# Performance work log

Measured on AMD Instinct MI355X. Metric: run time of the kernel, lower is better.

The kernel has to match this reference:

```python
import jax, jax.numpy as jnp
import numpy as np

N_NODES = 50000
N_EDGES = 1600000
D_EDGE = 64
D_NODE = 64
D_HID = 256
D_OUT = 64


def setup_inputs() -> dict:
    key = jax.random.key(0)
    ks = jax.random.split(key, 5)
    node_feats = jax.random.normal(ks[0], (N_NODES, D_NODE), dtype=jnp.float32)
    edge_feats = jax.random.normal(ks[1], (N_EDGES, D_EDGE), dtype=jnp.float32)
    receivers = jax.random.randint(ks[2], (N_EDGES,), 0, N_NODES, dtype=jnp.int64 if jax.config.jax_enable_x64 else jnp.int32)
    W1 = jax.random.normal(ks[3], (D_EDGE + D_NODE, D_HID), dtype=jnp.float32) * 0.05
    b1 = jnp.zeros((D_HID,), dtype=jnp.float32)
    W2 = jax.random.normal(ks[4], (D_HID, D_OUT), dtype=jnp.float32) * 0.05
    b2 = jnp.zeros((D_OUT,), dtype=jnp.float32)
    return {"node_feats": node_feats, "edge_feats": edge_feats, "receivers": receivers,
            "W1": W1, "b1": b1, "W2": W2, "b2": b2}


def reference(node_feats, edge_feats, receivers, W1, b1, W2, b2):
    # e2n aggregation: mean of incoming-edge features per node (segment mean),
    # faithful to gathering edata[G.incoming_edges(nid)] and averaging.
    n = node_feats.shape[0]
    agg_sum = jax.ops.segment_sum(edge_feats, receivers, num_segments=n)  # [N, De]
    counts = jax.ops.segment_sum(jnp.ones((edge_feats.shape[0],), edge_feats.dtype),
                                 receivers, num_segments=n)               # [N]
    agg = agg_sum / jnp.maximum(counts, 1.0)[:, None]
    # concat aggregated edge features with node features, then MLP updater
    x = jnp.concatenate([agg, node_feats], axis=1)                        # [N, De+Dv]
    h = jax.nn.relu(x @ W1 + b1)
    return h @ W2 + b2                                                    # [N, Dout]
```

## Files before the change

### kernel.cpp

```cpp
#include <hip/hip_runtime.h>

#define N_NODES 50000
#define N_EDGES 1600000
#define CAP 160

typedef short bf16x8 __attribute__((ext_vector_type(8)));
typedef float f32x4  __attribute__((ext_vector_type(4)));

__device__ inline unsigned f2bf(float f) {
    union { float f; unsigned u; } v; v.f = f;
    unsigned r = v.u + 0x7fff + ((v.u >> 16) & 1);
    return r >> 16;
}

__global__ __launch_bounds__(256) void zero_cursors_kernel(int* __restrict__ p) {
    int i = blockIdx.x * 256 + threadIdx.x;
    if (i < N_NODES) p[i] = 0;
}

__global__ __launch_bounds__(256) void bin_direct_kernel(
    const int* __restrict__ receivers,
    int* __restrict__ cursors,
    int* __restrict__ edge_ids)
{
    int e = blockIdx.x * 256 + threadIdx.x;
    if (e < N_EDGES) {
        int r = receivers[e];
        int p = atomicAdd(&cursors[r], 1);
        if (p < CAP) edge_ids[(size_t)r * CAP + p] = e;
    }
}

__global__ __launch_bounds__(256) void prepack_kernel(
    const float* __restrict__ W1, const float* __restrict__ W2,
    short* __restrict__ W1p, short* __restrict__ W2p)
{
    int t = blockIdx.x * 256 + threadIdx.x;
    if (t < 4096) {
        int c = (t >> 6) & 3, nt = t >> 8, l = t & 63;
        short tmp[8];
        #pragma unroll
        for (int j = 0; j < 8; ++j) {
            int k = c * 32 + (l >> 4) * 8 + j;
            tmp[j] = (short)f2bf(W1[k * 256 + nt * 16 + (l & 15)]);
        }
        #pragma unroll
        for (int j = 0; j < 8; ++j) W1p[(size_t)t * 8 + j] = tmp[j];
    } else if (t < 6144) {
        int u = t - 4096;
        int c = (u >> 6) & 7, nt = u >> 9, l = u & 63;
        short tmp[8];
        #pragma unroll
        for (int j = 0; j < 8; ++j) {
            int k = c * 32 + (l >> 4) * 8 + j;
            tmp[j] = (short)f2bf(W2[k * 64 + nt * 16 + (l & 15)]);
        }
        #pragma unroll
        for (int j = 0; j < 8; ++j) W2p[(size_t)u * 8 + j] = tmp[j];
    }
}

__global__ __launch_bounds__(512) void fused_gather_mlp_kernel(
    const float* __restrict__ edge_feats,
    const int*   __restrict__ edge_ids,
    const int*   __restrict__ counts,
    const float* __restrict__ node_feats,
    const short* __restrict__ W1p, const float* __restrict__ b1,
    const short* __restrict__ W2p, const float* __restrict__ b2,
    float*       __restrict__ out)
{
    __shared__ uint4 xbuf[512];
    __shared__ uint4 hbuf[1024];
    char* xb = (char*)xbuf;
    char* hb = (char*)hbuf;
    const int t = threadIdx.x;
    const int l = t & 63;
    const int w = t >> 6;
    const int g = l >> 4;
    const int q = l & 15;
    const int node0 = blockIdx.x * 32;

    {
        int node = t >> 4;
        int qq = t & 15;
        int nl = node0 + node;
        float4 v = make_float4(0.f, 0.f, 0.f, 0.f);
        if (nl < N_NODES) v = ((const float4*)(node_feats + (size_t)nl * 64))[qq];
        unsigned lo = f2bf(v.x) | (f2bf(v.y) << 16);
        unsigned hi = f2bf(v.z) | (f2bf(v.w) << 16);
        int byte = node * 256 + 128 + qq * 8;
        byte ^= (node & 7) << 4;
        *(uint2*)(xb + byte) = make_uint2(lo, hi);
    }

    for (int n = 0; n < 4; ++n) {
        int nodeLocal = w * 4 + n;
        int node = node0 + nodeLocal;
        int cnt = (node < N_NODES) ? min(counts[node], CAP) : 0;
        const int* ids = edge_ids + (size_t)node * CAP;
        float4 acc0 = make_float4(0.f, 0.f, 0.f, 0.f);
        float4 acc1 = make_float4(0.f, 0.f, 0.f, 0.f);
        for (int base = 0; base < cnt; base += 64) {
            int m = min(cnt - base, 64);
            int myid = (l < m) ? ids[base + l] : 0;
            for (int half = 0; half < m; half += 32) {
                #pragma unroll
                for (int u = 0; u < 8; ++u) {
                    int r = half + u * 4 + g;
                    int e = __shfl(myid, r);
                    if (r < m) {
                        float4 v = *((const float4*)(edge_feats + (size_t)e * 64) + q);
                        if (u & 1) { acc1.x += v.x; acc1.y += v.y;
                                     acc1.z += v.z; acc1.w += v.w; }
                        else       { acc0.x += v.x; acc0.y += v.y;
                                     acc0.z += v.z; acc0.w += v.w; }
                    }
                }
            }
        }
        float4 acc = make_float4(acc0.x + acc1.x, acc0.y + acc1.y,
                                 acc0.z + acc1.z, acc0.w + acc1.w);
        acc.x += __shfl_xor(acc.x, 16); acc.y += __shfl_xor(acc.y, 16);
        acc.z += __shfl_xor(acc.z, 16); acc.w += __shfl_xor(acc.w, 16);
        acc.x += __shfl_xor(acc.x, 32); acc.y += __shfl_xor(acc.y, 32);
        acc.z += __shfl_xor(acc.z, 32); acc.w += __shfl_xor(acc.w, 32);
        if (g == 0) {
            float inv = 1.f / fmaxf((float)cnt, 1.f);
            unsigned lo = f2bf(acc.x * inv) | (f2bf(acc.y * inv) << 16);
            unsigned hi = f2bf(acc.z * inv) | (f2bf(acc.w * inv) << 16);
            int byte = nodeLocal * 256 + q * 8;
            byte ^= (nodeLocal & 7) << 4;
            *(uint2*)(xb + byte) = make_uint2(lo, hi);
        }
    }
    __syncthreads();

    bf16x8 afr[2][4];
    #pragma unroll
    for (int m = 0; m < 2; ++m)
        #pragma unroll
        for (int c = 0; c < 4; ++c) {
            int row  = m * 16 + (l & 15);
            int byte = row * 256 + c * 64 + (l >> 4) * 16;
            byte ^= (row & 7) << 4;
            afr[m][c] = *(const bf16x8*)(xb + byte);
        }
    #pragma unroll
    for (int i = 0; i < 2; ++i) {
        int nt = w * 2 + i;
        bf16x8 bfr[4];
        #pragma unroll
        for (int c = 0; c < 4; ++c)
            bfr[c] = *(const bf16x8*)(W1p + ((size_t)(nt * 4 + c) * 64 + l) * 8);
        float bb = b1[nt * 16 + (l & 15)];
        #pragma unroll
        for (int m = 0; m < 2; ++m) {
            f32x4 acc = {0.f, 0.f, 0.f, 0.f};
            #pragma unroll
            for (int c = 0; c < 4; ++c)
                acc = __builtin_amdgcn_mfma_f32_16x16x32_bf16(afr[m][c], bfr[c], acc, 0, 0, 0);
            #pragma unroll
            for (int r = 0; r < 4; ++r) {
                int row = m * 16 + (l >> 4) * 4 + r;
                int col = nt * 16 + (l & 15);
                unsigned hv = f2bf(fmaxf(acc[r] + bb, 0.f));
                int byte = row * 512 + col * 2;
                byte ^= (row & 7) << 4;
                *(unsigned short*)(hb + byte) = (unsigned short)hv;
            }
        }
    }
    __syncthreads();

    {
        const int mt = w >> 2;
        const int nt = w & 3;
        bf16x8 a2[8];
        #pragma unroll
        for (int c = 0; c < 8; ++c) {
            int row  = mt * 16 + (l & 15);
            int byte = row * 512 + c * 64 + (l >> 4) * 16;
            byte ^= (row & 7) << 4;
            a2[c] = *(const bf16x8*)(hb + byte);
        }
        bf16x8 bfr[8];
        #pragma unroll
        for (int c = 0; c < 8; ++c)
            bfr[c] = *(const bf16x8*)(W2p + ((size_t)(nt * 8 + c) * 64 + l) * 8);
        f32x4 acc = {0.f, 0.f, 0.f, 0.f};
        #pragma unroll
        for (int c = 0; c < 8; ++c)
            acc = __builtin_amdgcn_mfma_f32_16x16x32_bf16(a2[c], bfr[c], acc, 0, 0, 0);
        float bb = b2[nt * 16 + (l & 15)];
        #pragma unroll
        for (int r = 0; r < 4; ++r) {
            int node = node0 + mt * 16 + (l >> 4) * 4 + r;
            if (node < N_NODES)
                out[(size_t)node * 64 + nt * 16 + (l & 15)] = acc[r] + bb;
        }
    }
}

__global__ __launch_bounds__(256) void scatter_kernel(
    const float* __restrict__ edge_feats, const int* __restrict__ receivers,
    float* __restrict__ agg, float* __restrict__ fcounts)
{
    int gid = blockIdx.x * 256 + threadIdx.x;
    int e = gid >> 6, d = gid & 63;
    if (e >= N_EDGES) return;
    int r = receivers[e];
    atomicAdd(&agg[(size_t)r * 64 + d], edge_feats[(size_t)e * 64 + d]);
    if (d == 0) atomicAdd(&fcounts[r], 1.0f);
}
__global__ __launch_bounds__(256) void normalize_kernel(
    float* __restrict__ agg, const float* __restrict__ fcounts)
{
    int i = blockIdx.x * 256 + threadIdx.x;
    if (i < N_NODES * 64) agg[i] /= fmaxf(fcounts[i >> 6], 1.0f);
}
__global__ __launch_bounds__(256) void mlp_f32_kernel(
    const float* __restrict__ node_feats,
    const float* __restrict__ W1, const float* __restrict__ b1,
    const float* __restrict__ W2, const float* __restrict__ b2,
    float*       __restrict__ agg_out)
{
    __shared__ float x[16][128];
    __shared__ float h[16][256];
    const int t = threadIdx.x;
    const int node0 = blockIdx.x * 16;
    for (int i = t; i < 2048; i += 256) {
        int n = i >> 7, k = i & 127;
        int node = node0 + n;
        float v = 0.f;
        if (node < N_NODES)
            v = (k < 64) ? agg_out[(size_t)node * 64 + k]
                         : node_feats[(size_t)node * 64 + (k - 64)];
        x[n][k] = v;
    }
    __syncthreads();
    {
        float acc[16];
        #pragma unroll
        for (int n = 0; n < 16; ++n) acc[n] = 0.f;
        for (int k = 0; k < 128; ++k) {
            float ww = W1[k * 256 + t];
            #pragma unroll
            for (int n = 0; n < 16; ++n) acc[n] += x[n][k] * ww;
        }
        float bb = b1[t];
        #pragma unroll
        for (int n = 0; n < 16; ++n) h[n][t] = fmaxf(acc[n] + bb, 0.f);
    }
    __syncthreads();
    {
        int c = t & 63, n0 = (t >> 6) * 4;
        float acc[4] = {0.f, 0.f, 0.f, 0.f};
        for (int k = 0; k < 256; ++k) {
            float ww = W2[k * 64 + c];
            #pragma unroll
            for (int i = 0; i < 4; ++i) acc[i] += h[n0 + i][k] * ww;
        }
        float bb = b2[c];
        #pragma unroll
        for (int i = 0; i < 4; ++i) {
            int node = node0 + n0 + i;
            if (node < N_NODES) agg_out[(size_t)node * 64 + c] = acc[i] + bb;
        }
    }
}

extern "C" void kernel_launch(void* const* d_in, const int* in_sizes, int n_in,
                              void* d_out, int out_size, void* d_ws, size_t ws_size,
                              hipStream_t stream) {
    const float* node_feats = (const float*)d_in[0];
    const float* edge_feats = (const float*)d_in[1];
    const int*   receivers  = (const int*)  d_in[2];
    const float* W1 = (const float*)d_in[3];
    const float* b1 = (const float*)d_in[4];
    const float* W2 = (const float*)d_in[5];
    const float* b2 = (const float*)d_in[6];
    float* out = (float*)d_out;

    char* wsc = (char*)d_ws;
    short* W1p     = (short*)wsc;
    short* W2p     = (short*)(wsc + 65536);
    int*   cursors = (int*)  (wsc + 98304);
    int*   edge_ids= cursors + N_NODES;
    size_t need = 98304 + (size_t)N_NODES * sizeof(int) * (1 + CAP);

    if (ws_size >= need) {
        prepack_kernel<<<24, 256, 0, stream>>>(W1, W2, W1p, W2p);
        zero_cursors_kernel<<<(N_NODES + 255) / 256, 256, 0, stream>>>(cursors);
        bin_direct_kernel<<<(N_EDGES + 255) / 256, 256, 0, stream>>>(
            receivers, cursors, edge_ids);
        fused_gather_mlp_kernel<<<(N_NODES + 31) / 32, 512, 0, stream>>>(
            edge_feats, edge_ids, cursors, node_feats, W1p, b1, W2p, b2, out);
    } else {
        float* fcounts = (float*)d_ws;
        hipMemsetAsync(d_out, 0, (size_t)N_NODES * 64 * sizeof(float), stream);
        hipMemsetAsync(fcounts, 0, N_NODES * sizeof(float), stream);
        scatter_kernel<<<(N_EDGES * 64) / 256, 256, 0, stream>>>(
            edge_feats, receivers, out, fcounts);
        normalize_kernel<<<(N_NODES * 64 + 255) / 256, 256, 0, stream>>>(out, fcounts);
        mlp_f32_kernel<<<(N_NODES + 15) / 16, 256, 0, stream>>>(
            node_feats, W1, b1, W2, b2, out);
    }
}
```

Measured before the change: 241.0 us.

## Permute edge features into per-node bf16 buckets before fused gather-MLP

Replaces edge-id binning with a permute kernel. It atomically assigns each edge a slot in its receiver's bucket and writes that edge's features there, converted to bf16. The fused gather-MLP kernel then streams contiguous bf16 rows per node instead of doing indirect fp32 row gathers through edge ids. This trades random gather reads for an extra full pass over edge features plus a scattered write into a roughly 1 GB bucket buffer. It also lowers the precision of the aggregated edge features, and the larger workspace requirement may send execution to the fallback path.

```diff
diff --git a/kernel.cpp b/kernel.cpp
--- a/kernel.cpp
+++ b/kernel.cpp
@@ -12,23 +12,16 @@
     unsigned r = v.u + 0x7fff + ((v.u >> 16) & 1);
     return r >> 16;
 }
+__device__ inline float bf2f_lo(unsigned u) {
+    union { unsigned u; float f; } v; v.u = u << 16; return v.f;
+}
+__device__ inline float bf2f_hi(unsigned u) {
+    union { unsigned u; float f; } v; v.u = u & 0xffff0000u; return v.f;
+}
 
 __global__ __launch_bounds__(256) void zero_cursors_kernel(int* __restrict__ p) {
     int i = blockIdx.x * 256 + threadIdx.x;
     if (i < N_NODES) p[i] = 0;
-}
-
-__global__ __launch_bounds__(256) void bin_direct_kernel(
-    const int* __restrict__ receivers,
-    int* __restrict__ cursors,
-    int* __restrict__ edge_ids)
-{
-    int e = blockIdx.x * 256 + threadIdx.x;
-    if (e < N_EDGES) {
-        int r = receivers[e];
-        int p = atomicAdd(&cursors[r], 1);
-        if (p < CAP) edge_ids[(size_t)r * CAP + p] = e;
-    }
 }
 
 __global__ __launch_bounds__(256) void prepack_kernel(
@@ -60,9 +53,37 @@
     }
 }
 
+__global__ __launch_bounds__(256) void permute_kernel(
+    const float* __restrict__ edge_feats,
+    const int*   __restrict__ receivers,
+    int*         __restrict__ cursors,
+    unsigned short* __restrict__ buckets)
+{
+    const int t = threadIdx.x;
+    const int l = t & 63;
+    const int g = l >> 4;
+    const int q = l & 15;
+    int wave   = (blockIdx.x * 256 + t) >> 6;
+    int nwaves = (gridDim.x * 256) >> 6;
+    for (int eg = wave; eg < N_EDGES / 4; eg += nwaves) {
+        int e0 = eg * 4;
+        int r = receivers[e0 + (l & 3)];
+        int p = 0;
+        if (l < 4) p = atomicAdd(&cursors[r], 1);
+        int slotv = r * CAP + p;
+        int okv   = (p < CAP) ? 1 : 0;
+        int slot_g = __shfl(slotv, g);
+        int ok_g   = __shfl(okv,   g);
+        float4 v = *(const float4*)(edge_feats + (size_t)(e0 + g) * 64 + q * 4);
+        unsigned lo = f2bf(v.x) | (f2bf(v.y) << 16);
+        unsigned hi = f2bf(v.z) | (f2bf(v.w) << 16);
+        if (ok_g)
+            *(uint2*)(buckets + (size_t)slot_g * 64 + q * 4) = make_uint2(lo, hi);
+    }
+}
+
 __global__ __launch_bounds__(512) void fused_gather_mlp_kernel(
-    const float* __restrict__ edge_feats,
-    const int*   __restrict__ edge_ids,
+    const unsigned short* __restrict__ buckets,
     const int*   __restrict__ counts,
     const float* __restrict__ node_feats,
     const short* __restrict__ W1p, const float* __restrict__ b1,
@@ -97,24 +118,21 @@
         int nodeLocal = w * 4 + n;
         int node = node0 + nodeLocal;
         int cnt = (node < N_NODES) ? min(counts[node], CAP) : 0;
-        const int* ids = edge_ids + (size_t)node * CAP;
+        const unsigned short* bk = buckets + (size_t)node * CAP * 64;
         float4 acc0 = make_float4(0.f, 0.f, 0.f, 0.f);
         float4 acc1 = make_float4(0.f, 0.f, 0.f, 0.f);
-        for (int base = 0; base < cnt; base += 64) {
-            int m = min(cnt - base, 64);
-            int myid = (l < m) ? ids[base + l] : 0;
-            for (int half = 0; half < m; half += 32) {
-                #pragma unroll
-                for (int u = 0; u < 8; ++u) {
-                    int r = half + u * 4 + g;
-                    int e = __shfl(myid, r);
-                    if (r < m) {
-                        float4 v = *((const float4*)(edge_feats + (size_t)e * 64) + q);
-                        if (u & 1) { acc1.x += v.x; acc1.y += v.y;
-                                     acc1.z += v.z; acc1.w += v.w; }
-                        else       { acc0.x += v.x; acc0.y += v.y;
-                                     acc0.z += v.z; acc0.w += v.w; }
-                    }
+        for (int i = 0; i < cnt; i += 16) {
+            #pragma unroll
+            for (int u = 0; u < 4; ++u) {
+                int r = i + u * 4 + g;
+                if (r < cnt) {
+                    uint2 v = *(const uint2*)(bk + (size_t)r * 64 + q * 4);
+                    float f0 = bf2f_lo(v.x), f1 = bf2f_hi(v.x);
+                    float f2 = bf2f_lo(v.y), f3 = bf2f_hi(v.y);
+                    if (u & 1) { acc1.x += f0; acc1.y += f1;
+                                 acc1.z += f2; acc1.w += f3; }
+                    else       { acc0.x += f0; acc0.y += f1;
+                                 acc0.z += f2; acc0.w += f3; }
                 }
             }
         }
@@ -285,16 +303,16 @@
     short* W1p     = (short*)wsc;
     short* W2p     = (short*)(wsc + 65536);
     int*   cursors = (int*)  (wsc + 98304);
-    int*   edge_ids= cursors + N_NODES;
-    size_t need = 98304 + (size_t)N_NODES * sizeof(int) * (1 + CAP);
+    unsigned short* buckets = (unsigned short*)(wsc + 298496);
+    size_t need = 298496 + (size_t)N_NODES * CAP * 64 * sizeof(unsigned short);
 
     if (ws_size >= need) {
         prepack_kernel<<<24, 256, 0, stream>>>(W1, W2, W1p, W2p);
         zero_cursors_kernel<<<(N_NODES + 255) / 256, 256, 0, stream>>>(cursors);
-        bin_direct_kernel<<<(N_EDGES + 255) / 256, 256, 0, stream>>>(
-            receivers, cursors, edge_ids);
+        permute_kernel<<<4096, 256, 0, stream>>>(
+            edge_feats, receivers, cursors, buckets);
         fused_gather_mlp_kernel<<<(N_NODES + 31) / 32, 512, 0, stream>>>(
-            edge_feats, edge_ids, cursors, node_feats, W1p, b1, W2p, b2, out);
+            buckets, cursors, node_feats, W1p, b1, W2p, b2, out);
     } else {
         float* fcounts = (float*)d_ws;
         hipMemsetAsync(d_out, 0, (size_t)N_NODES * 64 * sizeof(float), stream);
```

Result: faster. 213.7 us (-11.3%).

## Convert edge features to FP8 before the random gather in the fused kernel

Applied to the files above, without the earlier changes.

Adds a streaming kernel that converts the fp32 edge feature matrix to packed FP8 in workspace. The fused gather then reads 4 bytes per lane instead of 16, so random-access gather traffic drops by 4x. The trade is an extra full sequential read of the edge features plus a quarter-size write, and a large loss of precision in the mean aggregation that may exceed tolerance.

```diff
diff --git a/kernel.cpp b/kernel.cpp
--- a/kernel.cpp
+++ b/kernel.cpp
@@ -1,4 +1,5 @@
 #include <hip/hip_runtime.h>
+#include <hip/hip_fp16.h>
 
 #define N_NODES 50000
 #define N_EDGES 1600000
@@ -6,11 +7,42 @@
 
 typedef short bf16x8 __attribute__((ext_vector_type(8)));
 typedef float f32x4  __attribute__((ext_vector_type(4)));
+typedef float f32x2  __attribute__((ext_vector_type(2)));
+typedef unsigned u32x4 __attribute__((ext_vector_type(4)));
 
 __device__ inline unsigned f2bf(float f) {
     union { float f; unsigned u; } v; v.f = f;
     unsigned r = v.u + 0x7fff + ((v.u >> 16) & 1);
     return r >> 16;
+}
+
+__device__ inline unsigned pack_fp8x4(float a, float b, float c, float d) {
+#if __has_builtin(__builtin_amdgcn_cvt_pk_fp8_f32)
+    unsigned p = (unsigned)__builtin_amdgcn_cvt_pk_fp8_f32(a, b, 0, false);
+    p = (unsigned)__builtin_amdgcn_cvt_pk_fp8_f32(c, d, (int)p, true);
+    return p;
+#else
+    unsigned h, b0, b1, b2, b3;
+    h = __half_as_ushort(__float2half(a)); b0 = ((h + 0x7f + ((h >> 8) & 1)) >> 8) & 0xff;
+    h = __half_as_ushort(__float2half(b)); b1 = ((h + 0x7f + ((h >> 8) & 1)) >> 8) & 0xff;
+    h = __half_as_ushort(__float2half(c)); b2 = ((h + 0x7f + ((h >> 8) & 1)) >> 8) & 0xff;
+    h = __half_as_ushort(__float2half(d)); b3 = ((h + 0x7f + ((h >> 8) & 1)) >> 8) & 0xff;
+    return b0 | (b1 << 8) | (b2 << 16) | (b3 << 24);
+#endif
+}
+__device__ inline float4 unpack_fp8x4(unsigned u) {
+#if __has_builtin(__builtin_amdgcn_cvt_pk_f32_fp8)
+    f32x2 lo = __builtin_amdgcn_cvt_pk_f32_fp8((int)u, false);
+    f32x2 hi = __builtin_amdgcn_cvt_pk_f32_fp8((int)u, true);
+    return make_float4(lo[0], lo[1], hi[0], hi[1]);
+#else
+    __half_raw h0; h0.x = (unsigned short)((u & 0xff) << 8);
+    __half_raw h1; h1.x = (unsigned short)(((u >> 8) & 0xff) << 8);
+    __half_raw h2; h2.x = (unsigned short)(((u >> 16) & 0xff) << 8);
+    __half_raw h3; h3.x = (unsigned short)(((u >> 24) & 0xff) << 8);
+    return make_float4(__half2float(h0), __half2float(h1),
+                       __half2float(h2), __half2float(h3));
+#endif
 }
 
 __global__ __launch_bounds__(256) void zero_cursors_kernel(int* __restrict__ p) {
@@ -31,37 +63,30 @@
     }
 }
 
-__global__ __launch_bounds__(256) void prepack_kernel(
-    const float* __restrict__ W1, const float* __restrict__ W2,
-    short* __restrict__ W1p, short* __restrict__ W2p)
-{
-    int t = blockIdx.x * 256 + threadIdx.x;
-    if (t < 4096) {
-        int c = (t >> 6) & 3, nt = t >> 8, l = t & 63;
-        short tmp[8];
-        #pragma unroll
-        for (int j = 0; j < 8; ++j) {
-            int k = c * 32 + (l >> 4) * 8 + j;
-            tmp[j] = (short)f2bf(W1[k * 256 + nt * 16 + (l & 15)]);
-        }
-        #pragma unroll
-        for (int j = 0; j < 8; ++j) W1p[(size_t)t * 8 + j] = tmp[j];
-    } else if (t < 6144) {
-        int u = t - 4096;
-        int c = (u >> 6) & 7, nt = u >> 9, l = u & 63;
-        short tmp[8];
-        #pragma unroll
-        for (int j = 0; j < 8; ++j) {
-            int k = c * 32 + (l >> 4) * 8 + j;
-            tmp[j] = (short)f2bf(W2[k * 64 + nt * 16 + (l & 15)]);
-        }
-        #pragma unroll
-        for (int j = 0; j < 8; ++j) W2p[(size_t)u * 8 + j] = tmp[j];
+__global__ __launch_bounds__(256) void convert_fp8_kernel(
+    const float* __restrict__ src,
+    u32x4* __restrict__ dst)
+{
+    const int NQ = (N_EDGES * 64) / 16;
+    int idx = blockIdx.x * 256 + threadIdx.x;
+    int stride = gridDim.x * 256;
+    const f32x4* s4 = (const f32x4*)src;
+    for (int i = idx; i < NQ; i += stride) {
+        f32x4 a = __builtin_nontemporal_load(&s4[(size_t)i * 4 + 0]);
+        f32x4 b = __builtin_nontemporal_load(&s4[(size_t)i * 4 + 1]);
+        f32x4 c = __builtin_nontemporal_load(&s4[(size_t)i * 4 + 2]);
+        f32x4 d = __builtin_nontemporal_load(&s4[(size_t)i * 4 + 3]);
+        u32x4 o;
+        o[0] = pack_fp8x4(a[0], a[1], a[2], a[3]);
+        o[1] = pack_fp8x4(b[0], b[1], b[2], b[3]);
+        o[2] = pack_fp8x4(c[0], c[1], c[2], c[3]);
+        o[3] = pack_fp8x4(d[0], d[1], d[2], d[3]);
+        dst[i] = o;
     }
 }
 
 __global__ __launch_bounds__(512) void fused_gather_mlp_kernel(
-    const float* __restrict__ edge_feats,
+    const unsigned char* __restrict__ fp8e,
     const int*   __restrict__ edge_ids,
     const int*   __restrict__ counts,
     const float* __restrict__ node_feats,
@@ -109,11 +134,12 @@
                     int r = half + u * 4 + g;
                     int e = __shfl(myid, r);
                     if (r < m) {
-                        float4 v = *((const float4*)(edge_feats + (size_t)e * 64) + q);
-                        if (u & 1) { acc1.x += v.x; acc1.y += v.y;
-                                     acc1.z += v.z; acc1.w += v.w; }
-                        else       { acc0.x += v.x; acc0.y += v.y;
-                                     acc0.z += v.z; acc0.w += v.w; }
+                        unsigned uv = *(const unsigned*)(fp8e + (size_t)e * 64 + q * 4);
+                        float4 f = unpack_fp8x4(uv);
+                        if (u & 1) { acc1.x += f.x; acc1.y += f.y;
+                                     acc1.z += f.z; acc1.w += f.w; }
+                        else       { acc0.x += f.x; acc0.y += f.y;
+                                     acc0.z += f.z; acc0.w += f.w; }
                     }
                 }
             }
@@ -201,6 +227,35 @@
     }
 }
 
+__global__ __launch_bounds__(256) void prepack_kernel(
+    const float* __restrict__ W1, const float* __restrict__ W2,
+    short* __restrict__ W1p, short* __restrict__ W2p)
+{
+    int t = blockIdx.x * 256 + threadIdx.x;
+    if (t < 4096) {
+        int c = (t >> 6) & 3, nt = t >> 8, l = t & 63;
+        short tmp[8];
+        #pragma unroll
+        for (int j = 0; j < 8; ++j) {
+            int k = c * 32 + (l >> 4) * 8 + j;
+            tmp[j] = (short)f2bf(W1[k * 256 + nt * 16 + (l & 15)]);
+        }
+        #pragma unroll
+        for (int j = 0; j < 8; ++j) W1p[(size_t)t * 8 + j] = tmp[j];
+    } else if (t < 6144) {
+        int u = t - 4096;
+        int c = (u >> 6) & 7, nt = u >> 9, l = u & 63;
+        short tmp[8];
+        #pragma unroll
+        for (int j = 0; j < 8; ++j) {
+            int k = c * 32 + (l >> 4) * 8 + j;
+            tmp[j] = (short)f2bf(W2[k * 64 + nt * 16 + (l & 15)]);
+        }
+        #pragma unroll
+        for (int j = 0; j < 8; ++j) W2p[(size_t)u * 8 + j] = tmp[j];
+    }
+}
+
 __global__ __launch_bounds__(256) void scatter_kernel(
     const float* __restrict__ edge_feats, const int* __restrict__ receivers,
     float* __restrict__ agg, float* __restrict__ fcounts)
@@ -282,19 +337,24 @@
     float* out = (float*)d_out;
 
     char* wsc = (char*)d_ws;
-    short* W1p     = (short*)wsc;
-    short* W2p     = (short*)(wsc + 65536);
-    int*   cursors = (int*)  (wsc + 98304);
-    int*   edge_ids= cursors + N_NODES;
-    size_t need = 98304 + (size_t)N_NODES * sizeof(int) * (1 + CAP);
+    short* W1p      = (short*)wsc;
+    short* W2p      = (short*)(wsc + 65536);
+    int*   cursors  = (int*)  (wsc + 98304);
+    int*   edge_ids = (int*)  (wsc + 298496);
+    unsigned char* fp8e = (unsigned char*)(wsc + 298496 +
+                         (size_t)N_NODES * CAP * sizeof(int));
+    size_t need = 298496 + (size_t)N_NODES * CAP * sizeof(int)
+                + (size_t)N_EDGES * 64;
 
     if (ws_size >= need) {
         prepack_kernel<<<24, 256, 0, stream>>>(W1, W2, W1p, W2p);
         zero_cursors_kernel<<<(N_NODES + 255) / 256, 256, 0, stream>>>(cursors);
         bin_direct_kernel<<<(N_EDGES + 255) / 256, 256, 0, stream>>>(
             receivers, cursors, edge_ids);
+        convert_fp8_kernel<<<2048, 256, 0, stream>>>(
+            edge_feats, (u32x4*)fp8e);
         fused_gather_mlp_kernel<<<(N_NODES + 31) / 32, 512, 0, stream>>>(
-            edge_feats, edge_ids, cursors, node_feats, W1p, b1, W2p, b2, out);
+            fp8e, edge_ids, cursors, node_feats, W1p, b1, W2p, b2, out);
     } else {
         float* fcounts = (float*)d_ws;
         hipMemsetAsync(d_out, 0, (size_t)N_NODES * 64 * sizeof(float), stream);
```

After: 322.3 us. +33.7%, slower.
